# Performance work log

Hardware: AMD Instinct MI355X
Metric: run time of the kernel (lower is better)

## Reference

```python
import jax, jax.numpy as jnp
import numpy as np

N = 20000      # nodes
E = 640000     # edges (avg degree 32)
F = 128        # hidden_channels == num_filters
RBF = 64       # num_rbf
H = 8          # num_heads
DH = F // H    # head dim
T = 5          # number of distinct element types present in z
CUT = 5.0      # cutoff_upper (cutoff_lower = 0)


def setup_inputs() -> dict:
    key = jax.random.key(0)
    ks = jax.random.split(key, 20)
    s = 0.05
    inp = {
        "x": jax.random.normal(ks[0], (N, F), jnp.float32),
        "z": jax.random.randint(ks[1], (N,), 0, T, jnp.int32),
        "edge_index": jax.random.randint(ks[2], (2, E), 0, N, jnp.int32),
        "edge_weight": jax.random.uniform(ks[3], (E,), jnp.float32) * CUT,
        "edge_attr": jax.random.normal(ks[4], (E, RBF), jnp.float32),
        # ElemConv params
        "lin1_w": jax.random.normal(ks[5], (F, F), jnp.float32) / np.sqrt(F),
        "f_w1": jax.random.normal(ks[6], (F, RBF), jnp.float32) / np.sqrt(RBF),
        "f_b1": jnp.zeros((F,), jnp.float32),
        "f_w2": jax.random.normal(ks[7], (F, F), jnp.float32) / np.sqrt(F),
        "f_b2": jnp.zeros((F,), jnp.float32),
        # ElemAttn params
        "q_w": jax.random.normal(ks[8], (F, F), jnp.float32) / np.sqrt(F),
        "q_b": jax.random.normal(ks[9], (F,), jnp.float32) * s,
        "k_w": jax.random.normal(ks[10], (F, F), jnp.float32) / np.sqrt(F),
        "k_b": jax.random.normal(ks[11], (F,), jnp.float32) * s,
        "v_w": jax.random.normal(ks[12], (F, F), jnp.float32) / np.sqrt(F),
        "v_b": jax.random.normal(ks[13], (F,), jnp.float32) * s,
        "o1_w": jax.random.normal(ks[14], (F, F), jnp.float32) / np.sqrt(F),
        "o1_b": jax.random.normal(ks[15], (F,), jnp.float32) * s,
        "o2_w": jax.random.normal(ks[16], (F, F), jnp.float32) / np.sqrt(F),
        "o2_b": jax.random.normal(ks[17], (F,), jnp.float32) * s,
    }
    return inp


def reference(x, z, edge_index, edge_weight, edge_attr,
              lin1_w, f_w1, f_b1, f_w2, f_b2,
              q_w, q_b, k_w, k_b, v_w, v_b, o1_w, o1_b, o2_w, o2_b):
    silu = jax.nn.silu
    src, dst = edge_index[0], edge_index[1]

    # ---- ElemConv ----
    # CosineCutoff (cutoff_lower = 0)
    C = 0.5 * (jnp.cos(edge_weight * (jnp.pi / CUT)) + 1.0)
    C = C * (edge_weight < CUT).astype(x.dtype)
    # filter_net(edge_attr) * C
    W = silu(edge_attr @ f_w1.T + f_b1) @ f_w2.T + f_b2          # [E, F]
    W = W * C[:, None]
    xl = x @ lin1_w.T                                             # [N, F]
    msg = xl[src] * W                                             # [E, F]
    # aggregate by unique (z_j, dst) pair == dense [N, T] slot grid
    seg = dst * T + z[src]                                        # [E]
    y = jax.ops.segment_sum(msg, seg, num_segments=N * T).reshape(N, T, F)
    cnt = jax.ops.segment_sum(jnp.ones((E,), x.dtype), seg, num_segments=N * T)
    pm = (cnt > 0).astype(x.dtype).reshape(N, T)                  # presence mask

    # ---- ElemAttn (block-diagonal per target node over present slots) ----
    q = (y @ q_w.T + q_b).reshape(N, T, H, DH)
    k = (y @ k_w.T + k_b).reshape(N, T, H, DH)
    v = (y @ v_w.T + v_b).reshape(N, T, H, DH)
    attn = silu(jnp.einsum('nihd,njhd->nhij', q, k))              # [N, H, T, T]
    attn = attn * (pm[:, None, :, None] * pm[:, None, None, :])
    out = jnp.einsum('nhij,njhd->nihd', attn, v).reshape(N, T, F)
    out = out @ o1_w.T + o1_b                                     # [N, T, F]
    node = jnp.einsum('ntf,nt->nf', out, pm)                      # scatter-add by node
    return silu(node @ o2_w.T + o2_b)                             # [N, F]
```

## Files before the change

### kernel.cpp

```cpp
#include <hip/hip_runtime.h>

#define N_NODES 20000
#define E_EDGES 640000
#define F_DIM 128
#define RBF_DIM 64
#define T_TYPES 5
#define NSEG (N_NODES * T_TYPES)
#define EPB 128

typedef __attribute__((ext_vector_type(8))) short short8;
typedef __attribute__((ext_vector_type(4))) float f32x4;

__device__ __forceinline__ float silu_f(float x) { return x / (1.0f + __expf(-x)); }

__device__ __forceinline__ ushort f2bf(float f) {
  unsigned u = __float_as_uint(f);
  u += 0x7fffu + ((u >> 16) & 1u);
  return (ushort)(u >> 16);
}
__device__ __forceinline__ float bf2f(ushort u) {
  return __uint_as_float(((unsigned)u) << 16);
}
__device__ __forceinline__ unsigned cvt_pk(float lo, float hi) {
  unsigned r;
  asm("v_cvt_pk_bf16_f32 %0, %1, %2" : "=v"(r) : "v"(lo), "v"(hi));
  return r;
}
union S8U4 {
  short8 s;
  unsigned u[4];
};

__global__ __launch_bounds__(256) void prep_kernel(
    const float* __restrict__ w1, const float* __restrict__ w2,
    const float* __restrict__ qw, const float* __restrict__ kw,
    const float* __restrict__ vw, const float* __restrict__ o1w,
    const float* __restrict__ o2w, const float* __restrict__ lw,
    ushort* __restrict__ w1b, ushort* __restrict__ w2b,
    ushort* __restrict__ qwb, ushort* __restrict__ kwb,
    ushort* __restrict__ vwb, ushort* __restrict__ o1wb,
    ushort* __restrict__ o2wb, ushort* __restrict__ lwb,
    int* __restrict__ hist) {
  int i = blockIdx.x * 256 + threadIdx.x;
  if (i < F_DIM * RBF_DIM) w1b[i] = f2bf(w1[i]);
  if (i < F_DIM * F_DIM) {
    w2b[i] = f2bf(w2[i]);
    qwb[i] = f2bf(qw[i]);
    kwb[i] = f2bf(kw[i]);
    vwb[i] = f2bf(vw[i]);
    o1wb[i] = f2bf(o1w[i]);
    o2wb[i] = f2bf(o2w[i]);
    lwb[i] = f2bf(lw[i]);
  }
  for (int j = i; j < NSEG; j += 64 * 256) hist[j] = 0;
}

__global__ __launch_bounds__(256) void stage1_kernel(
    const int* __restrict__ srcp, const int* __restrict__ dstp,
    const int* __restrict__ z, int* __restrict__ hist, int* __restrict__ rnk,
    float* __restrict__ y, const float* __restrict__ x,
    const ushort* __restrict__ lwb, ushort* __restrict__ xlb) {
  const int b = blockIdx.x;
  const int tid = threadIdx.x;
  if (b < E_EDGES / 256) {
    int e = b * 256 + tid;
    int s = srcp[e];
    int seg = dstp[e] * T_TYPES + z[s];
    rnk[e] = atomicAdd(&hist[seg], 1);
    float4* yz = (float4*)(y + (size_t)b * 5120);
#pragma unroll
    for (int i = 0; i < 5; ++i)
      yz[tid + i * 256] = make_float4(0.f, 0.f, 0.f, 0.f);
  } else {
    const int lane = tid & 63;
    const int w = tid >> 6;
    const int lr = lane & 15, lh = lane >> 4;
    const int r0 = (b - E_EDGES / 256) * 80;

    f32x4 acc[5][2] = {};
#pragma unroll
    for (int ksi = 0; ksi < 4; ++ksi) {
      short8 B[2];
#pragma unroll
      for (int fc = 0; fc < 2; ++fc)
        B[fc] = *(const short8*)(lwb + (size_t)(w * 32 + fc * 16 + lr) * 128 +
                                 ksi * 32 + lh * 8);
#pragma unroll
      for (int fm = 0; fm < 5; ++fm) {
        const float* ap =
            x + (size_t)(r0 + fm * 16 + lr) * 128 + ksi * 32 + lh * 8;
        float4 a0 = *(const float4*)ap;
        float4 a1 = *(const float4*)(ap + 4);
        S8U4 t;
        t.u[0] = cvt_pk(a0.x, a0.y);
        t.u[1] = cvt_pk(a0.z, a0.w);
        t.u[2] = cvt_pk(a1.x, a1.y);
        t.u[3] = cvt_pk(a1.z, a1.w);
#pragma unroll
        for (int fc = 0; fc < 2; ++fc)
          acc[fm][fc] = __builtin_amdgcn_mfma_f32_16x16x32_bf16(
              t.s, B[fc], acc[fm][fc], 0, 0, 0);
      }
    }
#pragma unroll
    for (int fm = 0; fm < 5; ++fm)
#pragma unroll
      for (int fc = 0; fc < 2; ++fc)
#pragma unroll
        for (int rp = 0; rp < 4; rp += 2) {
          int rrow = fm * 16 + lh * 4 + rp;
          int col = w * 32 + fc * 16 + lr;
          unsigned u = cvt_pk(acc[fm][fc][rp], acc[fm][fc][rp + 1]);
          xlb[(size_t)(r0 + rrow) * 128 + col] = (ushort)u;
          xlb[(size_t)(r0 + rrow + 1) * 128 + col] = (ushort)(u >> 16);
        }
  }
}

__global__ __launch_bounds__(256) void scan1_kernel(const int* __restrict__ hist,
                                                    int* __restrict__ offs,
                                                    int* __restrict__ bsums) {
  __shared__ int lds[256];
  int tid = threadIdx.x;
  int base = blockIdx.x * 1024 + tid * 4;
  int v[4];
  int s = 0;
#pragma unroll
  for (int i = 0; i < 4; ++i) {
    v[i] = (base + i < NSEG) ? hist[base + i] : 0;
    s += v[i];
  }
  lds[tid] = s;
  __syncthreads();
  for (int d = 1; d < 256; d <<= 1) {
    int t = (tid >= d) ? lds[tid - d] : 0;
    __syncthreads();
    lds[tid] += t;
    __syncthreads();
  }
  int excl = lds[tid] - s;
#pragma unroll
  for (int i = 0; i < 4; ++i) {
    if (base + i < NSEG) offs[base + i] = excl;
    excl += v[i];
  }
  if (tid == 255) bsums[blockIdx.x] = lds[255];
}

__global__ __launch_bounds__(128) void scan2_kernel(int* __restrict__ bsums,
                                                    int nb) {
  __shared__ int lds[128];
  int tid = threadIdx.x;
  int v = (tid < nb) ? bsums[tid] : 0;
  lds[tid] = v;
  __syncthreads();
  for (int d = 1; d < 128; d <<= 1) {
    int t = (tid >= d) ? lds[tid - d] : 0;
    __syncthreads();
    lds[tid] += t;
    __syncthreads();
  }
  if (tid < nb) bsums[tid] = lds[tid] - v;
}

__global__ __launch_bounds__(256) void scatter_kernel(
    const int* __restrict__ srcp, const int* __restrict__ dstp,
    const int* __restrict__ z, const float* __restrict__ ewp,
    const int* __restrict__ offs, const int* __restrict__ bsums,
    const int* __restrict__ rnk, int* __restrict__ perm,
    int* __restrict__ ssegS, int* __restrict__ srcS,
    float* __restrict__ sCS) {
  int e = blockIdx.x * 256 + threadIdx.x;
  int s = srcp[e];
  int seg = dstp[e] * T_TYPES + z[s];
  int pos = offs[seg] + bsums[seg >> 10] + rnk[e];
  perm[pos] = e;
  ssegS[pos] = seg;
  srcS[pos] = s * 128;
  float wd = ewp[e];
  float c = 0.5f * (__cosf(wd * 0.6283185307179586f) + 1.0f);
  sCS[pos] = (wd < 5.0f) ? c : 0.0f;
}

__global__ __launch_bounds__(256, 4) void edge_mfma_kernel(
    const float* __restrict__ edge_attr, const int* __restrict__ perm,
    const int* __restrict__ ssegS, const int* __restrict__ srcS,
    const float* __restrict__ sCS, const ushort* __restrict__ w1b,
    const float* __restrict__ b1, const ushort* __restrict__ w2b,
    const float* __restrict__ b2, const ushort* __restrict__ xlb,
    float* __restrict__ y) {
  __shared__ ushort hs[128 * 136];
  __shared__ float sC[EPB];
  __shared__ int srcoff[EPB];
  __shared__ int sseg[EPB];
  __shared__ unsigned long long smask[2];

  const int tid = threadIdx.x;
  const int e0 = blockIdx.x * EPB;
  const int lane = tid & 63;
  const int w = tid >> 6;
  const int wm = w >> 1, wn = w & 1;
  const int lr = lane & 15, lh = lane >> 4;

  int prow[4];
#pragma unroll
  for (int fm = 0; fm < 4; ++fm) prow[fm] = perm[e0 + wm * 64 + fm * 16 + lr];

  float rb1[4], rb2[4];
#pragma unroll
  for (int fc = 0; fc < 4; ++fc) {
    int n = wn * 64 + fc * 16 + lr;
    rb1[fc] = b1[n];
    rb2[fc] = b2[n];
  }

  if (tid < EPB) {
    int p = e0 + tid;
    srcoff[tid] = srcS[p];
    sseg[tid] = ssegS[p];
    sC[tid] = sCS[p];
  }

  f32x4 acc[4][4] = {};
#pragma unroll
  for (int ks = 0; ks < 2; ++ks) {
    const int k0 = ks * 32;
    short8 af[4], bfr[4];
#pragma unroll
    for (int fm = 0; fm < 4; ++fm) {
      const float* ap = edge_attr + (size_t)prow[fm] * 64 + k0 + lh * 8;
      float4 a0 = *(const float4*)ap;
      float4 a1 = *(const float4*)(ap + 4);
      S8U4 t;
      t.u[0] = cvt_pk(a0.x, a0.y);
      t.u[1] = cvt_pk(a0.z, a0.w);
      t.u[2] = cvt_pk(a1.x, a1.y);
      t.u[3] = cvt_pk(a1.z, a1.w);
      af[fm] = t.s;
    }
#pragma unroll
    for (int fc = 0; fc < 4; ++fc)
      bfr[fc] = *(const short8*)(w1b + (size_t)(wn * 64 + fc * 16 + lr) * 64 +
                                 k0 + lh * 8);
#pragma unroll
    for (int fm = 0; fm < 4; ++fm)
#pragma unroll
      for (int fc = 0; fc < 4; ++fc)
        acc[fm][fc] = __builtin_amdgcn_mfma_f32_16x16x32_bf16(
            af[fm], bfr[fc], acc[fm][fc], 0, 0, 0);
  }

#pragma unroll
  for (int fm = 0; fm < 4; ++fm) {
#pragma unroll
    for (int fc = 0; fc < 4; ++fc) {
#pragma unroll
      for (int rp = 0; rp < 4; rp += 2) {
        int ml0 = wm * 64 + fm * 16 + lh * 4 + rp;
        int ml1 = ml0 + 1;
        int n = wn * 64 + fc * 16 + lr;
        float h0 = silu_f(acc[fm][fc][rp] + rb1[fc]);
        float h1 = silu_f(acc[fm][fc][rp + 1] + rb1[fc]);
        unsigned u = cvt_pk(h0, h1);
        hs[(ml0 * 256 + ((n * 2) ^ ((ml0 & 7) << 4))) >> 1] = (ushort)u;
        hs[(ml1 * 256 + ((n * 2) ^ ((ml1 & 7) << 4))) >> 1] = (ushort)(u >> 16);
      }
    }
  }
  __syncthreads();

  if (tid < EPB) {
    int head = (tid == 0) || (sseg[tid] != sseg[tid - 1]);
    unsigned long long m = __ballot(head);
    if ((tid & 63) == 0) smask[tid >> 6] = m;
  }

  f32x4 acc2[4][4] = {};
#pragma unroll
  for (int ks = 0; ks < 4; ++ks) {
    const int k0 = ks * 32;
    short8 af[4], bfr[4];
#pragma unroll
    for (int fm = 0; fm < 4; ++fm) {
      int ml = wm * 64 + fm * 16 + lr;
      int byte_in_row = (k0 * 2 + lh * 16) ^ ((ml & 7) << 4);
      af[fm] = *(const short8*)&hs[(ml * 256 + byte_in_row) >> 1];
    }
#pragma unroll
    for (int fc = 0; fc < 4; ++fc)
      bfr[fc] = *(const short8*)(w2b + (size_t)(wn * 64 + fc * 16 + lr) * 128 +
                                 k0 + lh * 8);
#pragma unroll
    for (int fm = 0; fm < 4; ++fm)
#pragma unroll
      for (int fc = 0; fc < 4; ++fc)
        acc2[fm][fc] = __builtin_amdgcn_mfma_f32_16x16x32_bf16(
            af[fm], bfr[fc], acc2[fm][fc], 0, 0, 0);
  }
  __syncthreads();

#pragma unroll
  for (int fm = 0; fm < 4; ++fm) {
#pragma unroll
    for (int rp = 0; rp < 4; rp += 2) {
      int ml0 = wm * 64 + fm * 16 + lh * 4 + rp;
      float c0 = sC[ml0], c1 = sC[ml0 + 1];
#pragma unroll
      for (int fc = 0; fc < 4; ++fc) {
        int n = wn * 64 + fc * 16 + lr;
        float v0 = (acc2[fm][fc][rp] + rb2[fc]) * c0;
        float v1 = (acc2[fm][fc][rp + 1] + rb2[fc]) * c1;
        *(unsigned*)&hs[n * 136 + ml0] = cvt_pk(v0, v1);
      }
    }
  }
  __syncthreads();

  {
    int cp = tid & 63;
    int q = tid >> 6;
    int rbase = q * 32;
    int c0 = cp * 2;
    unsigned mm = (unsigned)(smask[q >> 1] >> ((q & 1) * 32));
    float a0 = 0.0f, a1 = 0.0f;
    int cur = sseg[rbase];
    bool first = true;
#pragma unroll
    for (int it = 0; it < 4; ++it) {
      int r0 = rbase + it * 8;
      short8 m0 = *(const short8*)&hs[c0 * 136 + r0];
      short8 m1 = *(const short8*)&hs[(c0 + 1) * 136 + r0];
      unsigned xv[8];
#pragma unroll
      for (int j = 0; j < 8; ++j)
        xv[j] = *(const unsigned*)&xlb[(size_t)srcoff[r0 + j] + c0];
#pragma unroll
      for (int j = 0; j < 8; ++j) {
        int rr = it * 8 + j;
        if (rr && ((mm >> rr) & 1u)) {
          float* yp = &y[(size_t)cur * 128 + c0];
          if (first) {
            atomicAdd(yp, a0);
            atomicAdd(yp + 1, a1);
            first = false;
          } else {
            yp[0] = a0;
            yp[1] = a1;
          }
          a0 = a1 = 0.0f;
          cur = sseg[r0 + j];
        }
        a0 += bf2f((ushort)m0[j]) * bf2f((ushort)xv[j]);
        a1 += bf2f((ushort)m1[j]) * bf2f((ushort)(xv[j] >> 16));
      }
    }
    float* yp = &y[(size_t)cur * 128 + c0];
    atomicAdd(yp, a0);
    atomicAdd(yp + 1, a1);
  }
}

#define QS 136
#define NB 16
__global__ __launch_bounds__(256) void attn_out_kernel(
    const float* __restrict__ y, const int* __restrict__ hist,
    const ushort* __restrict__ qwb, const ushort* __restrict__ kwb,
    const ushort* __restrict__ vwb, const float* __restrict__ qb,
    const float* __restrict__ kb, const float* __restrict__ vb,
    const ushort* __restrict__ o1wb, const float* __restrict__ o1b,
    const ushort* __restrict__ o2wb, const float* __restrict__ o2b,
    float* __restrict__ outp) {
  __shared__ ushort bufA[80 * QS];
  __shared__ ushort bufB[80 * QS];
  __shared__ float aap[NB * 8 * 2 * 5];
  __shared__ float pmv[80];
  __shared__ float snpm[NB];
  __shared__ float sxb[3][128];

  const int tid = threadIdx.x;
  const int xcd = blockIdx.x & 7;
  const int loc = blockIdx.x >> 3;
  const int bid = (xcd < 2 ? xcd * 157 : 314 + (xcd - 2) * 156) + loc;
  const int n0 = bid * NB;
  const int row0 = n0 * T_TYPES;
  const int lane = tid & 63;
  const int w = tid >> 6;
  const int lr = lane & 15, lh = lane >> 4;

  if (tid < 128) {
    sxb[0][tid] = qb[tid];
    sxb[1][tid] = kb[tid];
    sxb[2][tid] = vb[tid];
  }
  if (tid < 80) pmv[tid] = (hist[(size_t)row0 + tid] > 0) ? 1.0f : 0.0f;

  short8 A[4][5];
#pragma unroll
  for (int ksi = 0; ksi < 4; ++ksi) {
#pragma unroll
    for (int fm = 0; fm < 5; ++fm) {
      const float* ap =
          y + (size_t)(row0 + fm * 16 + lr) * 128 + ksi * 32 + lh * 8;
      float4 a0 = *(const float4*)ap;
      float4 a1 = *(const float4*)(ap + 4);
      S8U4 t;
      t.u[0] = cvt_pk(a0.x, a0.y);
      t.u[1] = cvt_pk(a0.z, a0.w);
      t.u[2] = cvt_pk(a1.x, a1.y);
      t.u[3] = cvt_pk(a1.z, a1.w);
      A[ksi][fm] = t.s;
    }
  }
  __syncthreads();
  if (tid < NB) {
    float s = 0.0f;
#pragma unroll
    for (int t = 0; t < 5; ++t) s += pmv[tid * 5 + t];
    snpm[tid] = s;
  }

  auto do_proj = [&](const ushort* __restrict__ Wb, const float* bias_row,
                     ushort* __restrict__ dst) {
    f32x4 acc[5][2] = {};
#pragma unroll
    for (int ksi = 0; ksi < 4; ++ksi) {
      short8 B[2];
#pragma unroll
      for (int fc = 0; fc < 2; ++fc)
        B[fc] = *(const short8*)(Wb + (size_t)(w * 32 + fc * 16 + lr) * 128 +
                                 ksi * 32 + lh * 8);
#pragma unroll
      for (int fm = 0; fm < 5; ++fm)
#pragma unroll
        for (int fc = 0; fc < 2; ++fc)
          acc[fm][fc] = __builtin_amdgcn_mfma_f32_16x16x32_bf16(
              A[ksi][fm], B[fc], acc[fm][fc], 0, 0, 0);
    }
#pragma unroll
    for (int fm = 0; fm < 5; ++fm)
#pragma unroll
      for (int fc = 0; fc < 2; ++fc)
#pragma unroll
        for (int rp = 0; rp < 4; rp += 2) {
          int rrow = fm * 16 + lh * 4 + rp;
          int col = w * 32 + fc * 16 + lr;
          float v0 = acc[fm][fc][rp] + bias_row[col];
          float v1 = acc[fm][fc][rp + 1] + bias_row[col];
          unsigned u = cvt_pk(v0, v1);
          dst[rrow * QS + col] = (ushort)u;
          dst[(rrow + 1) * QS + col] = (ushort)(u >> 16);
        }
  };

  do_proj(qwb, sxb[0], bufA);
  do_proj(kwb, sxb[1], bufB);
  __syncthreads();

  {
    int n = tid >> 4, h = (tid >> 1) & 7, g = tid & 1;
    int i0 = g ? 3 : 0;
    int cnt = g ? 2 : 3;
    float kv[5][16];
#pragma unroll
    for (int j = 0; j < 5; ++j) {
      short8 v0 = *(const short8*)&bufB[(n * 5 + j) * QS + h * 16];
      short8 v1 = *(const short8*)&bufB[(n * 5 + j) * QS + h * 16 + 8];
#pragma unroll
      for (int d = 0; d < 8; ++d) {
        kv[j][d] = bf2f((ushort)v0[d]);
        kv[j][d + 8] = bf2f((ushort)v1[d]);
      }
    }
    float a[5] = {};
    for (int ii = 0; ii < cnt; ++ii) {
      int i = i0 + ii;
      float qv[16];
      short8 q0 = *(const short8*)&bufA[(n * 5 + i) * QS + h * 16];
      short8 q1 = *(const short8*)&bufA[(n * 5 + i) * QS + h * 16 + 8];
#pragma unroll
      for (int d = 0; d < 8; ++d) {
        qv[d] = bf2f((ushort)q0[d]);
        qv[d + 8] = bf2f((ushort)q1[d]);
      }
      float pmi = pmv[n * 5 + i];
#pragma unroll
      for (int j = 0; j < 5; ++j) {
        float dd = 0.0f;
#pragma unroll
        for (int d = 0; d < 16; ++d) dd += qv[d] * kv[j][d];
        a[j] += pmi * silu_f(dd);
      }
    }
#pragma unroll
    for (int j = 0; j < 5; ++j) aap[((n * 8 + h) * 2 + g) * 5 + j] = a[j];
  }
  __syncthreads();

  do_proj(vwb, sxb[2], bufA);
  __syncthreads();

  {
    int n = tid >> 4;
    int o = tid & 15;
    int f0 = o * 8;
    int h = f0 >> 4;
    float acc8[8] = {};
#pragma unroll
    for (int j = 0; j < 5; ++j) {
      float a = (aap[((n * 8 + h) * 2 + 0) * 5 + j] +
                 aap[((n * 8 + h) * 2 + 1) * 5 + j]) *
                pmv[n * 5 + j];
      short8 vv8 = *(const short8*)&bufA[(n * 5 + j) * QS + f0];
#pragma unroll
      for (int d = 0; d < 8; ++d) acc8[d] += a * bf2f((ushort)vv8[d]);
    }
    S8U4 t;
    t.u[0] = cvt_pk(acc8[0], acc8[1]);
    t.u[1] = cvt_pk(acc8[2], acc8[3]);
    t.u[2] = cvt_pk(acc8[4], acc8[5]);
    t.u[3] = cvt_pk(acc8[6], acc8[7]);
    *(short8*)&bufB[n * QS + f0] = t.s;
  }
  __syncthreads();

  {
    f32x4 acc[2] = {};
#pragma unroll
    for (int ksi = 0; ksi < 4; ++ksi) {
      short8 af = *(const short8*)&bufB[lr * QS + ksi * 32 + lh * 8];
      short8 B0 = *(const short8*)(o1wb + (size_t)(w * 32 + lr) * 128 +
                                   ksi * 32 + lh * 8);
      short8 B1 = *(const short8*)(o1wb + (size_t)(w * 32 + 16 + lr) * 128 +
                                   ksi * 32 + lh * 8);
      acc[0] = __builtin_amdgcn_mfma_f32_16x16x32_bf16(af, B0, acc[0], 0, 0, 0);
      acc[1] = __builtin_amdgcn_mfma_f32_16x16x32_bf16(af, B1, acc[1], 0, 0, 0);
    }
#pragma unroll
    for (int fc = 0; fc < 2; ++fc) {
      int col = w * 32 + fc * 16 + lr;
      float bb = o1b[col];
#pragma unroll
      for (int r = 0; r < 4; ++r) {
        int row = lh * 4 + r;
        bufA[row * QS + col] = f2bf(acc[fc][r] + snpm[row] * bb);
      }
    }
  }
  __syncthreads();

  {
    f32x4 acc[2] = {};
#pragma unroll
    for (int ksi = 0; ksi < 4; ++ksi) {
      short8 af = *(const short8*)&bufA[lr * QS + ksi * 32 + lh * 8];
      short8 B0 = *(const short8*)(o2wb + (size_t)(w * 32 + lr) * 128 +
                                   ksi * 32 + lh * 8);
      short8 B1 = *(const short8*)(o2wb + (size_t)(w * 32 + 16 + lr) * 128 +
                                   ksi * 32 + lh * 8);
      acc[0] = __builtin_amdgcn_mfma_f32_16x16x32_bf16(af, B0, acc[0], 0, 0, 0);
      acc[1] = __builtin_amdgcn_mfma_f32_16x16x32_bf16(af, B1, acc[1], 0, 0, 0);
    }
#pragma unroll
    for (int fc = 0; fc < 2; ++fc) {
      int col = w * 32 + fc * 16 + lr;
      float bb = o2b[col];
#pragma unroll
      for (int r = 0; r < 4; ++r) {
        int row = lh * 4 + r;
        outp[(size_t)(n0 + row) * 128 + col] = silu_f(acc[fc][r] + bb);
      }
    }
  }
}

extern "C" void kernel_launch(void* const* d_in, const int* in_sizes, int n_in,
                              void* d_out, int out_size, void* d_ws, size_t ws_size,
                              hipStream_t stream) {
  const float* x = (const float*)d_in[0];
  const int* z = (const int*)d_in[1];
  const int* ei = (const int*)d_in[2];
  const float* ew = (const float*)d_in[3];
  const float* ea = (const float*)d_in[4];
  const float* lin1_w = (const float*)d_in[5];
  const float* fw1 = (const float*)d_in[6];
  const float* fb1 = (const float*)d_in[7];
  const float* fw2 = (const float*)d_in[8];
  const float* fb2 = (const float*)d_in[9];
  const float* qw = (const float*)d_in[10];
  const float* qb = (const float*)d_in[11];
  const float* kw = (const float*)d_in[12];
  const float* kb = (const float*)d_in[13];
  const float* vw = (const float*)d_in[14];
  const float* vb = (const float*)d_in[15];
  const float* o1w = (const float*)d_in[16];
  const float* o1b = (const float*)d_in[17];
  const float* o2w = (const float*)d_in[18];
  const float* o2b = (const float*)d_in[19];
  float* outp = (float*)d_out;
  float* ws = (float*)d_ws;

  float* y = ws;
  ushort* xlb = (ushort*)(y + (size_t)NSEG * F_DIM);
  ushort* w1b = xlb + (size_t)N_NODES * F_DIM;
  ushort* w2b = w1b + F_DIM * RBF_DIM;
  ushort* qwb = w2b + F_DIM * F_DIM;
  ushort* kwb = qwb + F_DIM * F_DIM;
  ushort* vwb = kwb + F_DIM * F_DIM;
  ushort* o1wb = vwb + F_DIM * F_DIM;
  ushort* o2wb = o1wb + F_DIM * F_DIM;
  ushort* lwb = o2wb + F_DIM * F_DIM;
  int* hist = (int*)(lwb + F_DIM * F_DIM);
  int* offs = hist + NSEG;
  int* bsums = offs + NSEG;
  int* rnk = bsums + 128;
  int* perm = rnk + E_EDGES;
  int* ssegS = perm + E_EDGES;
  int* srcS = ssegS + E_EDGES;
  float* sCS = (float*)(srcS + E_EDGES);

  const int* srcp = ei;
  const int* dstp = ei + E_EDGES;
  const int NB_SCAN = (NSEG + 1023) / 1024;

  prep_kernel<<<64, 256, 0, stream>>>(fw1, fw2, qw, kw, vw, o1w, o2w, lin1_w,
                                      w1b, w2b, qwb, kwb, vwb, o1wb, o2wb, lwb,
                                      hist);
  stage1_kernel<<<E_EDGES / 256 + N_NODES / 80, 256, 0, stream>>>(
      srcp, dstp, z, hist, rnk, y, x, lwb, xlb);
  scan1_kernel<<<NB_SCAN, 256, 0, stream>>>(hist, offs, bsums);
  scan2_kernel<<<1, 128, 0, stream>>>(bsums, NB_SCAN);
  scatter_kernel<<<E_EDGES / 256, 256, 0, stream>>>(
      srcp, dstp, z, ew, offs, bsums, rnk, perm, ssegS, srcS, sCS);
  edge_mfma_kernel<<<E_EDGES / EPB, 256, 0, stream>>>(
      ea, perm, ssegS, srcS, sCS, w1b, fb1, w2b, fb2, xlb, y);
  attn_out_kernel<<<N_NODES / NB, 256, 0, stream>>>(y, hist, qwb, kwb, vwb, qb,
                                                    kb, vb, o1wb, o1b, o2wb,
                                                    o2b, outp);
}
```

Baseline: 292.2 us.

## Fold block-sum scan into scatter, repad LDS tile, raise MFMA wave priority

Removes the separate single-block scan2 launch by having every scatter block redundantly scan the 98 block sums in shared memory, which saves one kernel launch and its dependency gap. Changes the edge kernel's transposed LDS tile row stride from 136 to 132 shorts, which alters bank mapping and LDS footprint. Wraps the MFMA loops in the attention kernel with s_setprio to favour matrix-issuing waves. The redundant per-block scan adds barrier work to all 2500 scatter blocks, and the new stride may conflict differently on the packed writes.

```diff
diff --git a/kernel.cpp b/kernel.cpp
--- a/kernel.cpp
+++ b/kernel.cpp
@@ -7,6 +7,7 @@
 #define T_TYPES 5
 #define NSEG (N_NODES * T_TYPES)
 #define EPB 128
+#define MTS 132
 
 typedef __attribute__((ext_vector_type(8))) short short8;
 typedef __attribute__((ext_vector_type(4))) float f32x4;
@@ -147,22 +148,6 @@
   if (tid == 255) bsums[blockIdx.x] = lds[255];
 }
 
-__global__ __launch_bounds__(128) void scan2_kernel(int* __restrict__ bsums,
-                                                    int nb) {
-  __shared__ int lds[128];
-  int tid = threadIdx.x;
-  int v = (tid < nb) ? bsums[tid] : 0;
-  lds[tid] = v;
-  __syncthreads();
-  for (int d = 1; d < 128; d <<= 1) {
-    int t = (tid >= d) ? lds[tid - d] : 0;
-    __syncthreads();
-    lds[tid] += t;
-    __syncthreads();
-  }
-  if (tid < nb) bsums[tid] = lds[tid] - v;
-}
-
 __global__ __launch_bounds__(256) void scatter_kernel(
     const int* __restrict__ srcp, const int* __restrict__ dstp,
     const int* __restrict__ z, const float* __restrict__ ewp,
@@ -170,10 +155,25 @@
     const int* __restrict__ rnk, int* __restrict__ perm,
     int* __restrict__ ssegS, int* __restrict__ srcS,
     float* __restrict__ sCS) {
-  int e = blockIdx.x * 256 + threadIdx.x;
+  __shared__ int pb[128];
+  const int tid = threadIdx.x;
+  const int NB_SCAN = (NSEG + 1023) / 1024;
+  if (tid < 128) pb[tid] = (tid < NB_SCAN) ? bsums[tid] : 0;
+  __syncthreads();
+  int vown = (tid < 128) ? pb[tid] : 0;
+  for (int d = 1; d < 128; d <<= 1) {
+    int t = (tid >= d && tid < 128) ? pb[tid - d] : 0;
+    __syncthreads();
+    if (tid < 128) pb[tid] += t;
+    __syncthreads();
+  }
+  if (tid < 128) pb[tid] -= vown;
+  __syncthreads();
+
+  int e = blockIdx.x * 256 + tid;
   int s = srcp[e];
   int seg = dstp[e] * T_TYPES + z[s];
-  int pos = offs[seg] + bsums[seg >> 10] + rnk[e];
+  int pos = offs[seg] + pb[seg >> 10] + rnk[e];
   perm[pos] = e;
   ssegS[pos] = seg;
   srcS[pos] = s * 128;
@@ -189,7 +189,7 @@
     const float* __restrict__ b1, const ushort* __restrict__ w2b,
     const float* __restrict__ b2, const ushort* __restrict__ xlb,
     float* __restrict__ y) {
-  __shared__ ushort hs[128 * 136];
+  __shared__ ushort hs[128 * MTS];
   __shared__ float sC[EPB];
   __shared__ int srcoff[EPB];
   __shared__ int sseg[EPB];
@@ -310,7 +310,7 @@
         int n = wn * 64 + fc * 16 + lr;
         float v0 = (acc2[fm][fc][rp] + rb2[fc]) * c0;
         float v1 = (acc2[fm][fc][rp + 1] + rb2[fc]) * c1;
-        *(unsigned*)&hs[n * 136 + ml0] = cvt_pk(v0, v1);
+        *(unsigned*)&hs[n * MTS + ml0] = cvt_pk(v0, v1);
       }
     }
   }
@@ -328,8 +328,8 @@
 #pragma unroll
     for (int it = 0; it < 4; ++it) {
       int r0 = rbase + it * 8;
-      short8 m0 = *(const short8*)&hs[c0 * 136 + r0];
-      short8 m1 = *(const short8*)&hs[(c0 + 1) * 136 + r0];
+      short8 m0 = *(const short8*)&hs[c0 * MTS + r0];
+      short8 m1 = *(const short8*)&hs[(c0 + 1) * MTS + r0];
       unsigned xv[8];
 #pragma unroll
       for (int j = 0; j < 8; ++j)
@@ -422,6 +422,7 @@
   auto do_proj = [&](const ushort* __restrict__ Wb, const float* bias_row,
                      ushort* __restrict__ dst) {
     f32x4 acc[5][2] = {};
+    __builtin_amdgcn_s_setprio(1);
 #pragma unroll
     for (int ksi = 0; ksi < 4; ++ksi) {
       short8 B[2];
@@ -436,6 +437,7 @@
           acc[fm][fc] = __builtin_amdgcn_mfma_f32_16x16x32_bf16(
               A[ksi][fm], B[fc], acc[fm][fc], 0, 0, 0);
     }
+    __builtin_amdgcn_s_setprio(0);
 #pragma unroll
     for (int fm = 0; fm < 5; ++fm)
 #pragma unroll
@@ -525,6 +527,7 @@
 
   {
     f32x4 acc[2] = {};
+    __builtin_amdgcn_s_setprio(1);
 #pragma unroll
     for (int ksi = 0; ksi < 4; ++ksi) {
       short8 af = *(const short8*)&bufB[lr * QS + ksi * 32 + lh * 8];
@@ -535,6 +538,7 @@
       acc[0] = __builtin_amdgcn_mfma_f32_16x16x32_bf16(af, B0, acc[0], 0, 0, 0);
       acc[1] = __builtin_amdgcn_mfma_f32_16x16x32_bf16(af, B1, acc[1], 0, 0, 0);
     }
+    __builtin_amdgcn_s_setprio(0);
 #pragma unroll
     for (int fc = 0; fc < 2; ++fc) {
       int col = w * 32 + fc * 16 + lr;
@@ -550,6 +554,7 @@
 
   {
     f32x4 acc[2] = {};
+    __builtin_amdgcn_s_setprio(1);
 #pragma unroll
     for (int ksi = 0; ksi < 4; ++ksi) {
       short8 af = *(const short8*)&bufA[lr * QS + ksi * 32 + lh * 8];
@@ -560,6 +565,7 @@
       acc[0] = __builtin_amdgcn_mfma_f32_16x16x32_bf16(af, B0, acc[0], 0, 0, 0);
       acc[1] = __builtin_amdgcn_mfma_f32_16x16x32_bf16(af, B1, acc[1], 0, 0, 0);
     }
+    __builtin_amdgcn_s_setprio(0);
 #pragma unroll
     for (int fc = 0; fc < 2; ++fc) {
       int col = w * 32 + fc * 16 + lr;
@@ -628,7 +634,6 @@
   stage1_kernel<<<E_EDGES / 256 + N_NODES / 80, 256, 0, stream>>>(
       srcp, dstp, z, hist, rnk, y, x, lwb, xlb);
   scan1_kernel<<<NB_SCAN, 256, 0, stream>>>(hist, offs, bsums);
-  scan2_kernel<<<1, 128, 0, stream>>>(bsums, NB_SCAN);
   scatter_kernel<<<E_EDGES / 256, 256, 0, stream>>>(
       srcp, dstp, z, ew, offs, bsums, rnk, perm, ssegS, srcS, sCS);
   edge_mfma_kernel<<<E_EDGES / EPB, 256, 0, stream>>>(
```

Result: no change. 297.0 us (+1.7%).
